# Kernel tuning notes

Measured on AMD Instinct MI355X. Metric: run time of the kernel, lower is better.

## Reference

```python
import jax, jax.numpy as jnp
import numpy as np
import math


def setup_inputs() -> dict:
    key = jax.random.key(0)
    k_fm, k_x, k_y, k_w, k_h = jax.random.split(key, 5)
    C, H, W = 512, 256, 256
    N = 4096
    patch_num = 4
    pe = 2  # sqrt(patch_num)
    feature_map = jax.random.normal(k_fm, (C, H, W), dtype=jnp.float32)
    # Boxes fully inside the map with per-patch extent >= 2 so every sub-box is valid.
    min_wh = 2.0 * pe + 1.0
    x0 = jax.random.uniform(k_x, (N,), minval=0.0, maxval=W / 2 - 1.0)
    y0 = jax.random.uniform(k_y, (N,), minval=0.0, maxval=H / 2 - 1.0)
    w = jax.random.uniform(k_w, (N,), minval=min_wh, maxval=W / 2 - 2.0)
    h = jax.random.uniform(k_h, (N,), minval=min_wh, maxval=H / 2 - 2.0)
    roi_batch = jnp.stack([x0, y0, x0 + w, y0 + h], axis=1).astype(jnp.float32)
    return {"feature_map": feature_map, "roi_batch": roi_batch, "patch_num": patch_num}


def _box_indices(roi_batch, patch_num, W):
    """Rounded, clamped per-patch sub-box corners; shapes (P, N), flattened patch-major."""
    pe = int(math.isqrt(patch_num))
    xmin, ymin, xmax, ymax = (roi_batch[:, k] for k in range(4))
    i = jnp.arange(patch_num)
    ix = (i % pe).astype(roi_batch.dtype)[:, None]
    iy = (i // pe).astype(roi_batch.dtype)[:, None]
    ws = ((xmax - xmin) / pe)[None, :]
    hs = ((ymax - ymin) / pe)[None, :]
    ax = xmin[None, :] + ix * ws  # (P, N)
    ay = ymin[None, :] + iy * hs
    clampi = lambda v: jnp.clip(jnp.round(v), 0, W - 1).astype(jnp.int32)
    x0, x1 = clampi(ax), clampi(ax + ws)
    y0, y1 = clampi(ay), clampi(ay + hs)
    flat = lambda a: a.reshape(-1)  # loop order: patch outer, roi inner
    return flat(x0), flat(x1), flat(y0), flat(y1)


def reference(feature_map, roi_batch, patch_num):
    C, H, W = feature_map.shape
    x0, x1, y0, y1 = _box_indices(roi_batch, patch_num, W)
    cw = x1 - x0
    ch = y1 - y0
    mask = (cw >= 1) & (ch >= 1)  # (P*N,)
    # Integral image with zero row/col padding: S[:, y, x] = sum of fm[:, :y, :x]
    S = jnp.pad(jnp.cumsum(jnp.cumsum(feature_map, axis=1), axis=2),
                ((0, 0), (1, 0), (1, 0)))
    # Region sums via 4-corner gather: (C, B)
    sums = S[:, y1, x1] - S[:, y0, x1] - S[:, y1, x0] + S[:, y0, x0]
    area = jnp.maximum(cw * ch, 1).astype(feature_map.dtype)
    pooled = (sums / area).T  # (B, C) region means == adaptive_avg_pool2d(.,(1,1))
    pooled = pooled * mask.astype(feature_map.dtype)[:, None]
    return pooled[:, :, None, None], mask.astype(jnp.int32)
```

## Files before the change

### kernel.cpp

```cpp
#include <hip/hip_runtime.h>


#define CHN 512
#define HD  256
#define WD  256
#define SP  257
#define YC  8
#define NK  32
#define CB  32
#define OP_OFF 33817088UL

#define SIDX(cb, y, x)   ((((size_t)(cb) * SP + (y)) * SP + (x)) * CB)
#define OPIDX(cb, kk, x) ((((size_t)(cb) * 33 + (kk)) * SP + (x)) * CB)

typedef float f32x4 __attribute__((ext_vector_type(4)));

__device__ __forceinline__ void ntst4(float* p, float4 v) {
    f32x4 u;
    u.x = v.x; u.y = v.y; u.z = v.z; u.w = v.w;
    __builtin_nontemporal_store(u, (f32x4*)p);
}

#define BAR() do { asm volatile("s_waitcnt lgkmcnt(0)" ::: "memory"); \
                   __builtin_amdgcn_s_barrier(); \
                   asm volatile("" ::: "memory"); } while (0)

__global__ __launch_bounds__(512, 4) void fusedScanK(const float* __restrict__ fm,
                                                     float* __restrict__ S) {
    __shared__ float tile[2][CB][260];
    const int t = threadIdx.x, lane = t & 63, w = t >> 6;
    const int cb = blockIdx.x;
    const int c0 = cb * CB;
    const int k  = blockIdx.y;
    const int y0 = k * YC;

    const int cg = t & 7;
    const int x8 = t >> 3;
    const float4 z4 = make_float4(0.f, 0.f, 0.f, 0.f);

    if (k == 0) {
        #pragma unroll
        for (int it = 0; it < 4; ++it) {
            const int lin = it * 512 + t;
            const int cgg = lin & 7, x = lin >> 3;
            ntst4(S + SIDX(cb, 0, x) + 4 * cgg, z4);
        }
    }

    float4 cur[4], nxt[4];
    #pragma unroll
    for (int j = 0; j < 4; ++j)
        cur[j] = *(const float4*)(fm + ((size_t)(c0 + w * 4 + j) << 16)
                                     + (size_t)y0 * 256 + 4 * lane);

    float4 acc[4];
    #pragma unroll
    for (int m = 0; m < 4; ++m) acc[m] = z4;

    const int wcol = (4 * lane) ^ (4 * w);
    const int rxor = 4 * cg;

    for (int y = 0; y < YC; ++y) {
        const int buf = y & 1;
        if (y < YC - 1) {
            #pragma unroll
            for (int j = 0; j < 4; ++j)
                nxt[j] = *(const float4*)(fm + ((size_t)(c0 + w * 4 + j) << 16)
                                             + (size_t)(y0 + y + 1) * 256 + 4 * lane);
        }
        #pragma unroll
        for (int j = 0; j < 4; ++j) {
            const float4 v = cur[j];
            const float local = ((v.x + v.y) + v.z) + v.w;
            float s = local;
            #pragma unroll
            for (int d = 1; d < 64; d <<= 1) {
                float u = __shfl_up(s, d, 64);
                if (lane >= d) s += u;
            }
            const float e = s - local;
            float4 p;
            p.x = e   + v.x;
            p.y = p.x + v.y;
            p.z = p.y + v.z;
            p.w = p.z + v.w;
            *(float4*)&tile[buf][w * 4 + j][wcol] = p;
        }
        BAR();
        const size_t rowb = SIDX(cb, y0 + y + 1, 0);
        #pragma unroll
        for (int m = 0; m < 4; ++m) {
            const int x = x8 + 64 * m;
            const int xs = x ^ rxor;
            float4 a = acc[m];
            a.x += tile[buf][4 * cg + 0][xs];
            a.y += tile[buf][4 * cg + 1][xs];
            a.z += tile[buf][4 * cg + 2][xs];
            a.w += tile[buf][4 * cg + 3][xs];
            acc[m] = a;
            ntst4(S + rowb + (size_t)(x + 1) * CB + 4 * cg, a);
        }
        if (t < 8)
            ntst4(S + rowb + 4 * t, z4);
        #pragma unroll
        for (int j = 0; j < 4; ++j) cur[j] = nxt[j];
    }
}

__global__ __launch_bounds__(256) void offsetK(const float* __restrict__ S,
                                               float* __restrict__ OP) {
    const int gid = blockIdx.x * 256 + threadIdx.x;
    const int cc = gid & 31;
    const int xr = gid >> 5;
    const int x  = xr % SP;
    const int cb = xr / SP;
    OP[OPIDX(cb, 0, x) + cc] = 0.0f;
    OP[OPIDX(cb, 1, x) + cc] = 0.0f;
    double run = 0.0;
    #pragma unroll
    for (int j = 0; j < NK - 1; ++j) {
        run += (double)S[SIDX(cb, YC * (j + 1), x) + cc];
        OP[OPIDX(cb, j + 2, x) + cc] = (float)run;
    }
}

__global__ __launch_bounds__(256) void gatherK(const float* __restrict__ S,
                                              const float* __restrict__ OP,
                                              const float* __restrict__ roi,
                                              float* __restrict__ out,
                                              float* __restrict__ maskOut,
                                              int N) {
    const int n = blockIdx.x;
    const float xmin = roi[4 * n + 0];
    const float ymin = roi[4 * n + 1];
    const float xmax = roi[4 * n + 2];
    const float ymax = roi[4 * n + 3];

    const float wsv = __fdiv_rn(__fsub_rn(xmax, xmin), 2.0f);
    const float hsv = __fdiv_rn(__fsub_rn(ymax, ymin), 2.0f);
    const float ax1 = __fadd_rn(xmin, wsv);
    const float ay1 = __fadd_rn(ymin, hsv);
    const float lim = (float)(WD - 1);

    int rx[3], ry[3];
    rx[0] = (int)fminf(fmaxf(rintf(xmin), 0.0f), lim);
    rx[1] = (int)fminf(fmaxf(rintf(ax1), 0.0f), lim);
    rx[2] = (int)fminf(fmaxf(rintf(__fadd_rn(ax1, wsv)), 0.0f), lim);
    ry[0] = (int)fminf(fmaxf(rintf(ymin), 0.0f), lim);
    ry[1] = (int)fminf(fmaxf(rintf(ay1), 0.0f), lim);
    ry[2] = (int)fminf(fmaxf(rintf(__fadd_rn(ay1, hsv)), 0.0f), lim);

    const int t = threadIdx.x;
    const int cbb = t >> 4;
    const int cc  = (t & 15) * 2;
    float2 g[3][3];
    #pragma unroll
    for (int j = 0; j < 3; ++j) {
        const int kk = (ry[j] + YC - 1) >> 3;
        #pragma unroll
        for (int i = 0; i < 3; ++i) {
            const float2 l = *(const float2*)(S  + SIDX(cbb, ry[j], rx[i]) + cc);
            const float2 o = *(const float2*)(OP + OPIDX(cbb, kk, rx[i]) + cc);
            g[j][i] = make_float2(l.x + o.x, l.y + o.y);
        }
    }

    float m[4];
    #pragma unroll
    for (int p = 0; p < 4; ++p) {
        const int ix = p & 1, iy = p >> 1;
        const int cw = rx[ix + 1] - rx[ix];
        const int ch = ry[iy + 1] - ry[iy];
        const int maskv = (cw >= 1 && ch >= 1) ? 1 : 0;
        int areai = cw * ch; if (areai < 1) areai = 1;
        const float areaf = (float)areai;
        const float maskf = (float)maskv;
        m[p] = maskf;

        const float2 s11 = g[iy + 1][ix + 1];
        const float2 s01 = g[iy][ix + 1];
        const float2 s10 = g[iy + 1][ix];
        const float2 s00 = g[iy][ix];
        float2 o;
        o.x = __fdiv_rn(((s11.x - s01.x) - s10.x) + s00.x, areaf) * maskf;
        o.y = __fdiv_rn(((s11.y - s01.y) - s10.y) + s00.y, areaf) * maskf;
        *(float2*)(out + ((size_t)p * N + n) * CHN + 2 * t) = o;
    }
    if (t < 4) maskOut[(size_t)t * N + n] = m[t];
}

extern "C" void kernel_launch(void* const* d_in, const int* in_sizes, int n_in,
                              void* d_out, int out_size, void* d_ws, size_t ws_size,
                              hipStream_t stream) {
    const float* fm  = (const float*)d_in[0];
    const float* roi = (const float*)d_in[1];

    const int N = in_sizes[1] / 4;
    const int B = 4 * N;

    float* S  = (float*)d_ws;
    float* OP = (float*)d_ws + OP_OFF;
    float* out     = (float*)d_out;
    float* maskOut = out + (size_t)B * CHN;

    dim3 gF(CHN / CB, NK);
    fusedScanK<<<gF, 512, 0, stream>>>(fm, S);

    offsetK<<<(16 * SP * CB) / 256, 256, 0, stream>>>(S, OP);

    gatherK<<<N, 256, 0, stream>>>(S, OP, roi, out, maskOut, N);
}
```

Before: 270.1 us.

## Split channels into two halves so the integral image slice stays cache-resident

Processes the 512 channels in two 256-channel groups, running scan, offset and gather per group into a half-sized workspace, so each slice of the summed table (about 67MB) can sit in the large last-level cache for the gather. Stores to S become regular cached stores and feature-map loads become nontemporal, keeping the table in cache and streaming the input past it. The gather kernel now packs two ROIs per 256-thread block with 128 threads each and writes the mask only on the first pass. This doubles the kernel launches and may cut parallelism per launch.

Measured after the change: 246.6 us. -8.7%, faster.

```diff
diff --git a/kernel.cpp b/kernel.cpp
--- a/kernel.cpp
+++ b/kernel.cpp
@@ -2,23 +2,22 @@
 
 
 #define CHN 512
-#define HD  256
 #define WD  256
 #define SP  257
 #define YC  8
 #define NK  32
 #define CB  32
-#define OP_OFF 33817088UL
+#define GCH 256
+#define SLICE_OFF 16908544UL
 
 #define SIDX(cb, y, x)   ((((size_t)(cb) * SP + (y)) * SP + (x)) * CB)
 #define OPIDX(cb, kk, x) ((((size_t)(cb) * 33 + (kk)) * SP + (x)) * CB)
 
-typedef float f32x4 __attribute__((ext_vector_type(4)));
-
-__device__ __forceinline__ void ntst4(float* p, float4 v) {
-    f32x4 u;
-    u.x = v.x; u.y = v.y; u.z = v.z; u.w = v.w;
-    __builtin_nontemporal_store(u, (f32x4*)p);
+typedef float f32x4v __attribute__((ext_vector_type(4)));
+
+__device__ __forceinline__ float4 ntld4(const float* p) {
+    f32x4v u = __builtin_nontemporal_load((const f32x4v*)p);
+    return make_float4(u.x, u.y, u.z, u.w);
 }
 
 #define BAR() do { asm volatile("s_waitcnt lgkmcnt(0)" ::: "memory"); \
@@ -43,15 +42,15 @@
         for (int it = 0; it < 4; ++it) {
             const int lin = it * 512 + t;
             const int cgg = lin & 7, x = lin >> 3;
-            ntst4(S + SIDX(cb, 0, x) + 4 * cgg, z4);
+            *(float4*)(S + SIDX(cb, 0, x) + 4 * cgg) = z4;
         }
     }
 
     float4 cur[4], nxt[4];
     #pragma unroll
     for (int j = 0; j < 4; ++j)
-        cur[j] = *(const float4*)(fm + ((size_t)(c0 + w * 4 + j) << 16)
-                                     + (size_t)y0 * 256 + 4 * lane);
+        cur[j] = ntld4(fm + ((size_t)(c0 + w * 4 + j) << 16)
+                          + (size_t)y0 * 256 + 4 * lane);
 
     float4 acc[4];
     #pragma unroll
@@ -65,8 +64,8 @@
         if (y < YC - 1) {
             #pragma unroll
             for (int j = 0; j < 4; ++j)
-                nxt[j] = *(const float4*)(fm + ((size_t)(c0 + w * 4 + j) << 16)
-                                             + (size_t)(y0 + y + 1) * 256 + 4 * lane);
+                nxt[j] = ntld4(fm + ((size_t)(c0 + w * 4 + j) << 16)
+                                  + (size_t)(y0 + y + 1) * 256 + 4 * lane);
         }
         #pragma unroll
         for (int j = 0; j < 4; ++j) {
@@ -98,10 +97,10 @@
             a.z += tile[buf][4 * cg + 2][xs];
             a.w += tile[buf][4 * cg + 3][xs];
             acc[m] = a;
-            ntst4(S + rowb + (size_t)(x + 1) * CB + 4 * cg, a);
+            *(float4*)(S + rowb + (size_t)(x + 1) * CB + 4 * cg) = a;
         }
         if (t < 8)
-            ntst4(S + rowb + 4 * t, z4);
+            *(float4*)(S + rowb + 4 * t) = z4;
         #pragma unroll
         for (int j = 0; j < 4; ++j) cur[j] = nxt[j];
     }
@@ -129,8 +128,10 @@
                                               const float* __restrict__ roi,
                                               float* __restrict__ out,
                                               float* __restrict__ maskOut,
-                                              int N) {
-    const int n = blockIdx.x;
+                                              int N, int writeMask) {
+    const int t = threadIdx.x;
+    const int tl = t & 127;
+    const int n = blockIdx.x * 2 + (t >> 7);
     const float xmin = roi[4 * n + 0];
     const float ymin = roi[4 * n + 1];
     const float xmax = roi[4 * n + 2];
@@ -150,9 +151,8 @@
     ry[1] = (int)fminf(fmaxf(rintf(ay1), 0.0f), lim);
     ry[2] = (int)fminf(fmaxf(rintf(__fadd_rn(ay1, hsv)), 0.0f), lim);
 
-    const int t = threadIdx.x;
-    const int cbb = t >> 4;
-    const int cc  = (t & 15) * 2;
+    const int cbb = tl >> 4;
+    const int cc  = (tl & 15) * 2;
     float2 g[3][3];
     #pragma unroll
     for (int j = 0; j < 3; ++j) {
@@ -184,9 +184,9 @@
         float2 o;
         o.x = __fdiv_rn(((s11.x - s01.x) - s10.x) + s00.x, areaf) * maskf;
         o.y = __fdiv_rn(((s11.y - s01.y) - s10.y) + s00.y, areaf) * maskf;
-        *(float2*)(out + ((size_t)p * N + n) * CHN + 2 * t) = o;
-    }
-    if (t < 4) maskOut[(size_t)t * N + n] = m[t];
+        *(float2*)(out + ((size_t)p * N + n) * CHN + 2 * tl) = o;
+    }
+    if (writeMask && tl < 4) maskOut[(size_t)tl * N + n] = m[tl];
 }
 
 extern "C" void kernel_launch(void* const* d_in, const int* in_sizes, int n_in,
@@ -199,14 +199,19 @@
     const int B = 4 * N;
 
     float* S  = (float*)d_ws;
-    float* OP = (float*)d_ws + OP_OFF;
+    float* OP = (float*)d_ws + SLICE_OFF;
     float* out     = (float*)d_out;
     float* maskOut = out + (size_t)B * CHN;
 
-    dim3 gF(CHN / CB, NK);
-    fusedScanK<<<gF, 512, 0, stream>>>(fm, S);
-
-    offsetK<<<(16 * SP * CB) / 256, 256, 0, stream>>>(S, OP);
-
-    gatherK<<<N, 256, 0, stream>>>(S, OP, roi, out, maskOut, N);
-}
+    for (int g = 0; g < 2; ++g) {
+        const float* fm_g = fm + ((size_t)(g * GCH) << 16);
+        dim3 gF(GCH / CB, NK);
+        fusedScanK<<<gF, 512, 0, stream>>>(fm_g, S);
+
+        offsetK<<<(8 * SP * CB) / 256, 256, 0, stream>>>(S, OP);
+
+        gatherK<<<N / 2, 256, 0, stream>>>(S, OP, roi,
+                                           out + (size_t)g * GCH, maskOut,
+                                           N, g == 0 ? 1 : 0);
+    }
+}
```
